# Kernel optimization log

Measured on AMD Instinct MI355X. Metric: run time of the kernel, lower is better.

## Reference

```python
import jax, jax.numpy as jnp
import numpy as np
from jax import lax

C = 64
EPS = 1e-6

def ln2d(x, w, b):
    # channel-wise LN over HxW per (n, c)
    mean = x.mean(axis=(2, 3), keepdims=True)
    var = ((x - mean) ** 2).mean(axis=(2, 3), keepdims=True)
    return (x - mean) / jnp.sqrt(var + EPS) * w + b

def pw(x, w, b):
    # 1x1 conv: w [O, I], b [O]
    return jnp.einsum('nihw,oi->nohw', x, w) + b[None, :, None, None]

def dwconv3(x, w, b):
    # depthwise 3x3, w [2C, 1, 3, 3]
    y = lax.conv_general_dilated(x, w, window_strides=(1, 1), padding='SAME',
                                 feature_group_count=x.shape[1],
                                 dimension_numbers=('NCHW', 'OIHW', 'NCHW'))
    return y + b[None, :, None, None]

def simple_gate(x):
    x1, x2 = jnp.split(x, 2, axis=1)
    return x1 * x2

def setup_inputs() -> dict:
    key = jax.random.key(0)
    ks = jax.random.split(key, 16)
    s = 0.05
    return {
        'x': jax.random.normal(ks[0], (8, C, 256, 256), jnp.float32),
        'ln1_w': jnp.ones((1, C, 1, 1), jnp.float32),
        'ln1_b': jnp.zeros((1, C, 1, 1), jnp.float32),
        'pw1_w': jax.random.normal(ks[1], (2 * C, C), jnp.float32) * s,
        'pw1_b': jnp.zeros((2 * C,), jnp.float32),
        'dw_w': jax.random.normal(ks[2], (2 * C, 1, 3, 3), jnp.float32) * s,
        'dw_b': jnp.zeros((2 * C,), jnp.float32),
        'sca_w': jax.random.normal(ks[3], (C, C), jnp.float32) * s,
        'sca_b': jnp.zeros((C,), jnp.float32),
        'pw2_w': jax.random.normal(ks[4], (C, C), jnp.float32) * s,
        'pw2_b': jnp.zeros((C,), jnp.float32),
        'ln2_w': jnp.ones((1, C, 1, 1), jnp.float32),
        'ln2_b': jnp.zeros((1, C, 1, 1), jnp.float32),
        'pw3_w': jax.random.normal(ks[5], (2 * C, C), jnp.float32) * s,
        'pw3_b': jnp.zeros((2 * C,), jnp.float32),
        'pw4_w': jax.random.normal(ks[6], (C, C), jnp.float32) * s,
        'pw4_b': jnp.zeros((C,), jnp.float32),
        'beta1': jax.random.normal(ks[7], (1, C, 1, 1), jnp.float32) * 0.1,
        'beta2': jax.random.normal(ks[8], (1, C, 1, 1), jnp.float32) * 0.1,
    }

def reference(x, ln1_w, ln1_b, pw1_w, pw1_b, dw_w, dw_b, sca_w, sca_b,
              pw2_w, pw2_b, ln2_w, ln2_b, pw3_w, pw3_b, pw4_w, pw4_b,
              beta1, beta2):
    y = ln2d(x, ln1_w, ln1_b)
    y = pw(y, pw1_w, pw1_b)
    y = dwconv3(y, dw_w, dw_b)
    y = simple_gate(y)
    # SCA: global avg pool -> 1x1 conv -> sigmoid scale
    s = y.mean(axis=(2, 3), keepdims=True)          # [N, C, 1, 1]
    w = jax.nn.sigmoid(pw(s, sca_w, sca_b))
    y = y * w
    y = pw(y, pw2_w, pw2_b)
    x = x + beta1 * y
    y2 = ln2d(x, ln2_w, ln2_b)
    y2 = pw(y2, pw3_w, pw3_b)
    y2 = simple_gate(y2)
    y2 = pw(y2, pw4_w, pw4_b)
    return x + beta2 * y2
```

## Files before the change

kernel.cpp:

```cpp
#include <hip/hip_runtime.h>
#include <hip/hip_bf16.h>

#define NB 8
#define HWP 65536
#define ZS  65664
#define TS  65664
#define XS  65600

typedef __attribute__((ext_vector_type(8))) short short8;
typedef __attribute__((ext_vector_type(4))) float f32x4;

__device__ __forceinline__ short f2bf(float f) {
  union { float f; unsigned u; } v; v.f = f;
  return (short)((v.u + 0x7FFF + ((v.u >> 16) & 1)) >> 16);
}
__device__ __forceinline__ float bf2f(unsigned short u) {
  union { unsigned u; float f; } v; v.u = ((unsigned)u) << 16; return v.f;
}

__global__ __launch_bounds__(512) void ln_stats_kernel(
    const float* __restrict__ x, const float* __restrict__ lw,
    const float* __restrict__ lb, float* __restrict__ a, float* __restrict__ b) {
  int plane = blockIdx.x;
  int c = plane & 63;
  const float4* p4 = (const float4*)(x + (size_t)plane * HWP);
  float s = 0.f, s2 = 0.f;
  for (int i = threadIdx.x; i < HWP / 4; i += 512) {
    float4 v = p4[i];
    s  += v.x + v.y + v.z + v.w;
    s2 += v.x * v.x + v.y * v.y + v.z * v.z + v.w * v.w;
  }
  for (int off = 32; off; off >>= 1) {
    s  += __shfl_down(s, off);
    s2 += __shfl_down(s2, off);
  }
  __shared__ float ls[8], ls2[8];
  int wid = threadIdx.x >> 6, lid = threadIdx.x & 63;
  if (lid == 0) { ls[wid] = s; ls2[wid] = s2; }
  __syncthreads();
  if (threadIdx.x == 0) {
    float S = 0.f, S2 = 0.f;
    for (int k = 0; k < 8; k++) { S += ls[k]; S2 += ls2[k]; }
    float mean = S * (1.f / (float)HWP);
    float var  = S2 * (1.f / (float)HWP) - mean * mean;
    float rstd = rsqrtf(var + 1e-6f);
    float av = rstd * lw[c];
    a[plane] = av;
    b[plane] = lb[c] - mean * av;
  }
}

__global__ void fold_kernel(const float* __restrict__ w, const float* __restrict__ pb,
                            const float* __restrict__ a, const float* __restrict__ b,
                            unsigned short* __restrict__ wf16, float* __restrict__ cf, int O) {
  int idx = blockIdx.x * blockDim.x + threadIdx.x;
  if (idx >= NB * O) return;
  int n = idx / O, o = idx - n * O;
  int MT = O >> 4;
  const float* an = a + n * 64;
  const float* bn = b + n * 64;
  const float* wo = w + o * 64;
  int mt = o >> 4, cl = o & 15;
  float cc = pb[o];
  for (int i = 0; i < 64; i++) {
    float wv = wo[i];
    float wf = wv * an[i];
    cc += wv * bn[i];
    int ks = i >> 5, quad = (i >> 3) & 3, j = i & 7;
    wf16[((((size_t)(n * MT + mt) * 2 + ks) * 16 + cl) * 4 + quad) * 8 + j] =
        (unsigned short)f2bf(wf);
  }
  cf[idx] = cc;
}

__global__ void fold4_kernel(const float* __restrict__ w4, const float* __restrict__ pb4,
                             const float* __restrict__ beta2,
                             unsigned short* __restrict__ wf16, float* __restrict__ cf) {
  int o = threadIdx.x;
  if (o >= 64) return;
  float bt = beta2[o];
  int mt = o >> 4, cl = o & 15;
  for (int i = 0; i < 64; i++) {
    int ks = i >> 5, quad = (i >> 3) & 3, j = i & 7;
    wf16[((((size_t)mt * 2 + ks) * 16 + cl) * 4 + quad) * 8 + j] =
        (unsigned short)f2bf(bt * w4[o * 64 + i]);
  }
  cf[o] = bt * pb4[o];
}

__global__ __launch_bounds__(256, 2) void gemm_pw1_kernel(
    const float* __restrict__ x, const unsigned short* __restrict__ wf16,
    const float* __restrict__ cf, unsigned short* __restrict__ z) {
  int n = blockIdx.y;
  int lane = threadIdx.x & 63, wid = threadIdx.x >> 6;
  int col = lane & 15, quad = lane >> 4;
  const short8* wv8 = (const short8*)wf16 + (size_t)n * 1024;
  short8 a[8][2];
  #pragma unroll
  for (int mt = 0; mt < 8; mt++)
    #pragma unroll
    for (int ks = 0; ks < 2; ks++)
      a[mt][ks] = wv8[((mt * 2 + ks) * 16 + col) * 4 + quad];
  f32x4 cb[8];
  #pragma unroll
  for (int mt = 0; mt < 8; mt++)
    cb[mt] = *(const f32x4*)(cf + n * 128 + mt * 16 + quad * 4);
  const float* xn = x + (size_t)n * 64 * HWP;
  unsigned short* zn = z + (size_t)n * 128 * ZS;
  int pxbase = blockIdx.x * 128 + wid * 16 + col;

  auto load_b = [&](int p, short8* bf) {
    #pragma unroll
    for (int ks = 0; ks < 2; ks++) {
      short8 v;
      #pragma unroll
      for (int j = 0; j < 8; j++)
        v[j] = f2bf(xn[(size_t)(ks * 32 + quad * 8 + j) * HWP + p]);
      bf[ks] = v;
    }
  };

  short8 bb[2][2];
  load_b(pxbase, bb[0]);
  #pragma unroll
  for (int tile = 0; tile < 2; tile++) {
    int cur = tile & 1, nxt = cur ^ 1;
    int p = pxbase + tile * 64;
    if (tile < 1) load_b(p + 64, bb[nxt]);
    f32x4 acc[8];
    #pragma unroll
    for (int mt = 0; mt < 8; mt++) {
      acc[mt] = cb[mt];
      acc[mt] = __builtin_amdgcn_mfma_f32_16x16x32_bf16(a[mt][0], bb[cur][0], acc[mt], 0, 0, 0);
      acc[mt] = __builtin_amdgcn_mfma_f32_16x16x32_bf16(a[mt][1], bb[cur][1], acc[mt], 0, 0, 0);
    }
    #pragma unroll
    for (int mt = 0; mt < 8; mt++)
      #pragma unroll
      for (int r = 0; r < 4; r++)
        zn[(size_t)(mt * 16 + quad * 4 + r) * ZS + p] =
            (unsigned short)f2bf(acc[mt][r]);
  }
}

__global__ __launch_bounds__(256) void dwgate_kernel(
    const unsigned short* __restrict__ z, const float* __restrict__ dww,
    const float* __restrict__ dwb, unsigned short* __restrict__ t,
    float* __restrict__ pooled4) {
  int blk = blockIdx.x;
  int plane = blk >> 2, qtr = blk & 3;
  int n = plane >> 6, c = plane & 63;
  int lane = threadIdx.x & 63, wv = threadIdx.x >> 6;
  const unsigned short* z0 = z + ((size_t)n * 128 + c) * ZS;
  const unsigned short* z1 = z0 + (size_t)64 * ZS;
  unsigned short* tp = t + (size_t)plane * TS;
  float w0[9], w1[9];
  #pragma unroll
  for (int k = 0; k < 9; k++) { w0[k] = dww[c * 9 + k]; w1[k] = dww[(c + 64) * 9 + k]; }
  float bias0 = dwb[c], bias1 = dwb[c + 64];
  int r0 = qtr * 64 + wv * 16;
  int colb = lane * 4;

  float fa[3][4], la[3], ra[3];
  float fb[3][4], lb_[3], rb[3];

  auto loadrow = [&](const unsigned short* base, int h, float* f, float& l, float& r) {
    if ((unsigned)h < 256u) {
      ushort4 u = *(const ushort4*)(base + h * 256 + colb);
      f[0] = bf2f(u.x); f[1] = bf2f(u.y); f[2] = bf2f(u.z); f[3] = bf2f(u.w);
    } else {
      f[0] = f[1] = f[2] = f[3] = 0.f;
    }
    float ll = __shfl_up(f[3], 1);
    float rr = __shfl_down(f[0], 1);
    l = (lane == 0) ? 0.f : ll;
    r = (lane == 63) ? 0.f : rr;
  };

  loadrow(z0, r0 - 1, fa[0], la[0], ra[0]);
  loadrow(z1, r0 - 1, fb[0], lb_[0], rb[0]);
  loadrow(z0, r0,     fa[1], la[1], ra[1]);
  loadrow(z1, r0,     fb[1], lb_[1], rb[1]);

  float lsum = 0.f;
  #pragma unroll 2
  for (int h = r0; h < r0 + 16; h++) {
    loadrow(z0, h + 1, fa[2], la[2], ra[2]);
    loadrow(z1, h + 1, fb[2], lb_[2], rb[2]);
    float o0[4] = {bias0, bias0, bias0, bias0};
    float o1[4] = {bias1, bias1, bias1, bias1};
    #pragma unroll
    for (int rr_ = 0; rr_ < 3; rr_++) {
      float wl0 = w0[rr_ * 3], wc0 = w0[rr_ * 3 + 1], wr0 = w0[rr_ * 3 + 2];
      float wl1 = w1[rr_ * 3], wc1 = w1[rr_ * 3 + 1], wr1 = w1[rr_ * 3 + 2];
      const float* f0 = fa[rr_]; const float* f1 = fb[rr_];
      float l0 = la[rr_], r0h = ra[rr_], l1 = lb_[rr_], r1h = rb[rr_];
      o0[0] += wl0 * l0    + wc0 * f0[0] + wr0 * f0[1];
      o0[1] += wl0 * f0[0] + wc0 * f0[1] + wr0 * f0[2];
      o0[2] += wl0 * f0[1] + wc0 * f0[2] + wr0 * f0[3];
      o0[3] += wl0 * f0[2] + wc0 * f0[3] + wr0 * r0h;
      o1[0] += wl1 * l1    + wc1 * f1[0] + wr1 * f1[1];
      o1[1] += wl1 * f1[0] + wc1 * f1[1] + wr1 * f1[2];
      o1[2] += wl1 * f1[1] + wc1 * f1[2] + wr1 * f1[3];
      o1[3] += wl1 * f1[2] + wc1 * f1[3] + wr1 * r1h;
    }
    float g0 = o0[0] * o1[0], g1 = o0[1] * o1[1];
    float g2 = o0[2] * o1[2], g3 = o0[3] * o1[3];
    uint2 pk;
    pk.x = (unsigned)(unsigned short)f2bf(g0) | ((unsigned)(unsigned short)f2bf(g1) << 16);
    pk.y = (unsigned)(unsigned short)f2bf(g2) | ((unsigned)(unsigned short)f2bf(g3) << 16);
    *(uint2*)(tp + (size_t)h * 256 + colb) = pk;
    lsum += (g0 + g1) + (g2 + g3);
    #pragma unroll
    for (int i = 0; i < 4; i++) { fa[0][i] = fa[1][i]; fa[1][i] = fa[2][i];
                                  fb[0][i] = fb[1][i]; fb[1][i] = fb[2][i]; }
    la[0] = la[1]; la[1] = la[2]; ra[0] = ra[1]; ra[1] = ra[2];
    lb_[0] = lb_[1]; lb_[1] = lb_[2]; rb[0] = rb[1]; rb[1] = rb[2];
  }
  for (int off = 32; off; off >>= 1) lsum += __shfl_down(lsum, off);
  __shared__ float ls[4];
  if (lane == 0) ls[wv] = lsum;
  __syncthreads();
  if (threadIdx.x == 0) pooled4[plane * 4 + qtr] = ls[0] + ls[1] + ls[2] + ls[3];
}

__global__ __launch_bounds__(256) void sca_fold_kernel(
    const float* __restrict__ pooled4, const float* __restrict__ sw,
    const float* __restrict__ sb, const float* __restrict__ w2,
    const float* __restrict__ pb2, const float* __restrict__ beta1,
    unsigned short* __restrict__ wf16, float* __restrict__ cf) {
  __shared__ float scal[4][64];
  int ln = threadIdx.x >> 6, o = threadIdx.x & 63;
  int n = blockIdx.x * 4 + ln;
  const float* pm = pooled4 + n * 256;
  float s = sb[o];
  for (int i = 0; i < 64; i++)
    s += sw[o * 64 + i] * (pm[i * 4] + pm[i * 4 + 1] + pm[i * 4 + 2] + pm[i * 4 + 3]) *
         (1.f / 65536.f);
  scal[ln][o] = 1.f / (1.f + expf(-s));
  __syncthreads();
  float bt = beta1[o];
  int mt = o >> 4, cl = o & 15;
  for (int i = 0; i < 64; i++) {
    float wf = bt * w2[o * 64 + i] * scal[ln][i];
    int ks = i >> 5, quad = (i >> 3) & 3, j = i & 7;
    wf16[((((size_t)(n * 4 + mt) * 2 + ks) * 16 + cl) * 4 + quad) * 8 + j] =
        (unsigned short)f2bf(wf);
  }
  cf[n * 64 + o] = bt * pb2[o];
}

__global__ __launch_bounds__(256, 2) void gemm_pw2_kernel(
    const unsigned short* __restrict__ t, const float* __restrict__ x,
    const unsigned short* __restrict__ wf16, const float* __restrict__ cf,
    float* __restrict__ x1, float* __restrict__ part_sum, float* __restrict__ part_sq) {
  __shared__ float red_s[4][64], red_q[4][64];
  int n = blockIdx.y;
  int lane = threadIdx.x & 63, wid = threadIdx.x >> 6;
  int col = lane & 15, quad = lane >> 4;
  const short8* wv8 = (const short8*)wf16 + (size_t)n * 512;
  short8 a[4][2];
  #pragma unroll
  for (int mt = 0; mt < 4; mt++)
    #pragma unroll
    for (int ks = 0; ks < 2; ks++)
      a[mt][ks] = wv8[((mt * 2 + ks) * 16 + col) * 4 + quad];
  f32x4 cb[4];
  #pragma unroll
  for (int mt = 0; mt < 4; mt++)
    cb[mt] = *(const f32x4*)(cf + n * 64 + mt * 16 + quad * 4);
  const unsigned short* tn = t + (size_t)n * 64 * TS;
  const float* xn = x + (size_t)n * 64 * HWP;
  float* x1n = x1 + (size_t)n * 64 * XS;
  int pxbase = blockIdx.x * 128 + wid * 16 + col;

  auto load_t = [&](int p, short8* bf) {
    #pragma unroll
    for (int ks = 0; ks < 2; ks++) {
      short8 v;
      #pragma unroll
      for (int j = 0; j < 8; j++)
        v[j] = (short)tn[(size_t)(ks * 32 + quad * 8 + j) * TS + p];
      bf[ks] = v;
    }
  };
  auto load_x = [&](int p, float (*xv)[4]) {
    #pragma unroll
    for (int mt = 0; mt < 4; mt++)
      #pragma unroll
      for (int r = 0; r < 4; r++)
        xv[mt][r] = xn[(size_t)(mt * 16 + quad * 4 + r) * HWP + p];
  };

  float sacc[4][4], qacc[4][4];
  #pragma unroll
  for (int mt = 0; mt < 4; mt++)
    #pragma unroll
    for (int r = 0; r < 4; r++) { sacc[mt][r] = 0.f; qacc[mt][r] = 0.f; }

  short8 bb[2][2];
  float xv[2][4][4];
  load_t(pxbase, bb[0]);
  load_x(pxbase, xv[0]);
  #pragma unroll
  for (int tile = 0; tile < 2; tile++) {
    int cur = tile & 1, nxt = cur ^ 1;
    int p = pxbase + tile * 64;
    if (tile < 1) { load_t(p + 64, bb[nxt]); load_x(p + 64, xv[nxt]); }
    f32x4 acc[4];
    #pragma unroll
    for (int mt = 0; mt < 4; mt++) {
      acc[mt] = cb[mt];
      acc[mt] = __builtin_amdgcn_mfma_f32_16x16x32_bf16(a[mt][0], bb[cur][0], acc[mt], 0, 0, 0);
      acc[mt] = __builtin_amdgcn_mfma_f32_16x16x32_bf16(a[mt][1], bb[cur][1], acc[mt], 0, 0, 0);
    }
    #pragma unroll
    for (int mt = 0; mt < 4; mt++)
      #pragma unroll
      for (int r = 0; r < 4; r++) {
        size_t idx = (size_t)(mt * 16 + quad * 4 + r) * XS + p;
        float v = xv[cur][mt][r] + acc[mt][r];
        x1n[idx] = v;
        sacc[mt][r] += v;
        qacc[mt][r] += v * v;
      }
  }
  #pragma unroll
  for (int mt = 0; mt < 4; mt++)
    #pragma unroll
    for (int r = 0; r < 4; r++) {
      float s = sacc[mt][r], q = qacc[mt][r];
      #pragma unroll
      for (int off = 1; off < 16; off <<= 1) {
        s += __shfl_xor(s, off);
        q += __shfl_xor(q, off);
      }
      if (col == 0) {
        int o = mt * 16 + quad * 4 + r;
        red_s[wid][o] = s; red_q[wid][o] = q;
      }
    }
  __syncthreads();
  if (threadIdx.x < 64) {
    int c = threadIdx.x;
    float s = red_s[0][c] + red_s[1][c] + red_s[2][c] + red_s[3][c];
    float q = red_q[0][c] + red_q[1][c] + red_q[2][c] + red_q[3][c];
    size_t pidx = ((size_t)n * 64 + c) * 512 + blockIdx.x;
    part_sum[pidx] = s;
    part_sq[pidx]  = q;
  }
}

__global__ __launch_bounds__(256) void ln2fold_kernel(
    const float* __restrict__ w, const float* __restrict__ pb,
    const float* __restrict__ ps, const float* __restrict__ pq,
    const float* __restrict__ lw, const float* __restrict__ lb,
    unsigned short* __restrict__ wf16, float* __restrict__ cf) {
  __shared__ float aa[64], bbv[64];
  int n = blockIdx.x;
  int c = threadIdx.x >> 2, k4 = threadIdx.x & 3;
  const float* p1 = ps + ((size_t)n * 64 + c) * 512 + k4 * 128;
  const float* p2 = pq + ((size_t)n * 64 + c) * 512 + k4 * 128;
  float S = 0.f, S2 = 0.f;
  for (int k = 0; k < 128; k++) { S += p1[k]; S2 += p2[k]; }
  S  += __shfl_xor(S, 1);  S  += __shfl_xor(S, 2);
  S2 += __shfl_xor(S2, 1); S2 += __shfl_xor(S2, 2);
  if (k4 == 0) {
    float mean = S * (1.f / (float)HWP);
    float var  = S2 * (1.f / (float)HWP) - mean * mean;
    float rstd = rsqrtf(var + 1e-6f);
    float av = rstd * lw[c];
    aa[c] = av;
    bbv[c] = lb[c] - mean * av;
  }
  __syncthreads();
  if (threadIdx.x < 128) {
    int o = threadIdx.x;
    const float* wo = w + o * 64;
    int mt = o >> 4, cl = o & 15;
    float cc = pb[o];
    for (int i = 0; i < 64; i++) {
      float wv = wo[i];
      float wf = wv * aa[i];
      cc += wv * bbv[i];
      int ks = i >> 5, quad = (i >> 3) & 3, j = i & 7;
      wf16[((((size_t)(n * 8 + mt) * 2 + ks) * 16 + cl) * 4 + quad) * 8 + j] =
          (unsigned short)f2bf(wf);
    }
    cf[n * 128 + o] = cc;
  }
}

__global__ __launch_bounds__(256, 2) void final_mfma_kernel(
    const float* __restrict__ x1, const unsigned short* __restrict__ w3f16,
    const float* __restrict__ c3f, const unsigned short* __restrict__ w4f16,
    const float* __restrict__ c4f, float* __restrict__ out) {
  __shared__ float s_c3[128];
  __shared__ __align__(16) float s_c4[64];
  int n = blockIdx.y;
  int lane = threadIdx.x & 63, wid = threadIdx.x >> 6;
  int col = lane & 15, quad = lane >> 4;
  if (threadIdx.x < 128) s_c3[threadIdx.x] = c3f[n * 128 + threadIdx.x];
  if (threadIdx.x < 64) s_c4[threadIdx.x] = c4f[threadIdx.x];
  const short8* w3v = (const short8*)w3f16 + (size_t)n * 1024;
  short8 a3[8][2];
  #pragma unroll
  for (int mt = 0; mt < 8; mt++)
    #pragma unroll
    for (int ks = 0; ks < 2; ks++)
      a3[mt][ks] = w3v[((mt * 2 + ks) * 16 + col) * 4 + quad];
  const short8* w4v = (const short8*)w4f16;
  short8 a4[4][2];
  #pragma unroll
  for (int mt = 0; mt < 4; mt++)
    #pragma unroll
    for (int ks = 0; ks < 2; ks++)
      a4[mt][ks] = w4v[((mt * 2 + ks) * 16 + col) * 4 + quad];
  __syncthreads();
  const float* x1n = x1 + (size_t)n * 64 * XS;
  float* outn = out + (size_t)n * 64 * HWP;
  int pxbase = blockIdx.x * 128 + wid * 16 + col;

  auto load_b1 = [&](int p, short8* bf) {
    #pragma unroll
    for (int ks = 0; ks < 2; ks++) {
      short8 v;
      #pragma unroll
      for (int j = 0; j < 8; j++)
        v[j] = f2bf(x1n[(size_t)(ks * 32 + quad * 8 + j) * XS + p]);
      bf[ks] = v;
    }
  };

  short8 bb1[2][2];
  load_b1(pxbase, bb1[0]);
  #pragma unroll
  for (int tile = 0; tile < 2; tile++) {
    int cur = tile & 1, nxt = cur ^ 1;
    int p = pxbase + tile * 64;
    if (tile < 1) load_b1(p + 64, bb1[nxt]);
    f32x4 acc[8];
    #pragma unroll
    for (int mt = 0; mt < 8; mt++) {
      acc[mt] = (f32x4){0.f, 0.f, 0.f, 0.f};
      acc[mt] = __builtin_amdgcn_mfma_f32_16x16x32_bf16(a3[mt][0], bb1[cur][0], acc[mt], 0, 0, 0);
      acc[mt] = __builtin_amdgcn_mfma_f32_16x16x32_bf16(a3[mt][1], bb1[cur][1], acc[mt], 0, 0, 0);
    }
    unsigned pd[4][2];
    #pragma unroll
    for (int mt = 0; mt < 4; mt++)
      #pragma unroll
      for (int u = 0; u < 2; u++) {
        int c0 = mt * 16 + quad * 4 + 2 * u;
        float ga = (acc[mt][2 * u]     + s_c3[c0])     * (acc[mt + 4][2 * u]     + s_c3[64 + c0]);
        float gb = (acc[mt][2 * u + 1] + s_c3[c0 + 1]) * (acc[mt + 4][2 * u + 1] + s_c3[64 + c0 + 1]);
        pd[mt][u] = (unsigned)(unsigned short)f2bf(ga) |
                    ((unsigned)(unsigned short)f2bf(gb) << 16);
      }
    short8 b2f[2];
    #pragma unroll
    for (int ks = 0; ks < 2; ks++)
      #pragma unroll
      for (int w = 0; w < 4; w++) {
        int src = ((quad & 1) * 2 + (w >> 1)) * 16 + col;
        unsigned v0 = (unsigned)__shfl((int)pd[ks * 2][w & 1], src, 64);
        unsigned v1 = (unsigned)__shfl((int)pd[ks * 2 + 1][w & 1], src, 64);
        unsigned u = (quad & 2) ? v1 : v0;
        b2f[ks][2 * w]     = (short)(u & 0xFFFFu);
        b2f[ks][2 * w + 1] = (short)(u >> 16);
      }
    f32x4 acc2[4];
    #pragma unroll
    for (int mt = 0; mt < 4; mt++) {
      acc2[mt] = *(const f32x4*)&s_c4[mt * 16 + quad * 4];
      acc2[mt] = __builtin_amdgcn_mfma_f32_16x16x32_bf16(a4[mt][0], b2f[0], acc2[mt], 0, 0, 0);
      acc2[mt] = __builtin_amdgcn_mfma_f32_16x16x32_bf16(a4[mt][1], b2f[1], acc2[mt], 0, 0, 0);
    }
    #pragma unroll
    for (int mt = 0; mt < 4; mt++)
      #pragma unroll
      for (int r = 0; r < 4; r++) {
        size_t idx = (size_t)(mt * 16 + quad * 4 + r) * XS + p;
        outn[(size_t)(mt * 16 + quad * 4 + r) * HWP + p] = x1n[idx] + acc2[mt][r];
      }
  }
}

extern "C" void kernel_launch(void* const* d_in, const int* in_sizes, int n_in,
                              void* d_out, int out_size, void* d_ws, size_t ws_size,
                              hipStream_t stream) {
  const float* x    = (const float*)d_in[0];
  const float* ln1w = (const float*)d_in[1];
  const float* ln1b = (const float*)d_in[2];
  const float* pw1w = (const float*)d_in[3];
  const float* pw1b = (const float*)d_in[4];
  const float* dww  = (const float*)d_in[5];
  const float* dwb  = (const float*)d_in[6];
  const float* scaw = (const float*)d_in[7];
  const float* scab = (const float*)d_in[8];
  const float* pw2w = (const float*)d_in[9];
  const float* pw2b = (const float*)d_in[10];
  const float* ln2w = (const float*)d_in[11];
  const float* ln2b = (const float*)d_in[12];
  const float* pw3w = (const float*)d_in[13];
  const float* pw3b = (const float*)d_in[14];
  const float* pw4w = (const float*)d_in[15];
  const float* pw4b = (const float*)d_in[16];
  const float* beta1= (const float*)d_in[17];
  const float* beta2= (const float*)d_in[18];
  float* out = (float*)d_out;

  char* ws = (char*)d_ws;
  unsigned short* z  = (unsigned short*)ws;
  float*          x1 = (float*)ws;
  unsigned short* t  = (unsigned short*)(ws + 134479872ull);
  float* sm = (float*)(ws + 134479872ull + 67239936ull);
  float* a1 = sm;
  float* b1 = a1 + 512;
  float* c1f = b1 + 512;
  float* pooled4 = c1f + 1024;
  float* c2f = pooled4 + 2048;
  float* c3f = c2f + 512;
  float* c4f = c3f + 1024;
  unsigned short* w1f16 = (unsigned short*)(c4f + 64);
  unsigned short* w2f16 = w1f16 + 65536;
  unsigned short* w3f16 = w2f16 + 32768;
  unsigned short* w4f16 = w3f16 + 65536;
  float* part_sum = (float*)d_out;
  float* part_sq  = part_sum + 262144;

  hipLaunchKernelGGL(ln_stats_kernel, dim3(512), dim3(512), 0, stream, x, ln1w, ln1b, a1, b1);
  hipLaunchKernelGGL(fold_kernel, dim3(4), dim3(256), 0, stream, pw1w, pw1b, a1, b1, w1f16, c1f, 128);
  hipLaunchKernelGGL(fold4_kernel, dim3(1), dim3(64), 0, stream, pw4w, pw4b, beta2, w4f16, c4f);
  hipLaunchKernelGGL(gemm_pw1_kernel, dim3(512, 8), dim3(256), 0, stream, x, w1f16, c1f, z);
  hipLaunchKernelGGL(dwgate_kernel, dim3(2048), dim3(256), 0, stream, z, dww, dwb, t, pooled4);
  hipLaunchKernelGGL(sca_fold_kernel, dim3(2), dim3(256), 0, stream,
                     pooled4, scaw, scab, pw2w, pw2b, beta1, w2f16, c2f);
  hipLaunchKernelGGL(gemm_pw2_kernel, dim3(512, 8), dim3(256), 0, stream, t, x, w2f16, c2f, x1,
                     part_sum, part_sq);
  hipLaunchKernelGGL(ln2fold_kernel, dim3(8), dim3(256), 0, stream,
                     pw3w, pw3b, part_sum, part_sq, ln2w, ln2b, w3f16, c3f);
  hipLaunchKernelGGL(final_mfma_kernel, dim3(512, 8), dim3(256), 0, stream,
                     x1, w3f16, c3f, w4f16, c4f, out);
}
```

Measured before the change: 562.2 us.

## Switch intermediates z, t, x1 to pixel-major channel-last layout

```diff
diff --git a/kernel.cpp b/kernel.cpp
--- a/kernel.cpp
+++ b/kernel.cpp
@@ -3,9 +3,6 @@
 
 #define NB 8
 #define HWP 65536
-#define ZS  65664
-#define TS  65664
-#define XS  65600
 
 typedef __attribute__((ext_vector_type(8))) short short8;
 typedef __attribute__((ext_vector_type(4))) float f32x4;
@@ -106,7 +103,7 @@
   for (int mt = 0; mt < 8; mt++)
     cb[mt] = *(const f32x4*)(cf + n * 128 + mt * 16 + quad * 4);
   const float* xn = x + (size_t)n * 64 * HWP;
-  unsigned short* zn = z + (size_t)n * 128 * ZS;
+  unsigned short* zn = z + (size_t)n * HWP * 128;
   int pxbase = blockIdx.x * 128 + wid * 16 + col;
 
   auto load_b = [&](int p, short8* bf) {
@@ -135,108 +132,103 @@
       acc[mt] = __builtin_amdgcn_mfma_f32_16x16x32_bf16(a[mt][1], bb[cur][1], acc[mt], 0, 0, 0);
     }
     #pragma unroll
-    for (int mt = 0; mt < 8; mt++)
-      #pragma unroll
-      for (int r = 0; r < 4; r++)
-        zn[(size_t)(mt * 16 + quad * 4 + r) * ZS + p] =
-            (unsigned short)f2bf(acc[mt][r]);
+    for (int mt = 0; mt < 8; mt++) {
+      uint2 pk;
+      pk.x = (unsigned)(unsigned short)f2bf(acc[mt][0]) |
+             ((unsigned)(unsigned short)f2bf(acc[mt][1]) << 16);
+      pk.y = (unsigned)(unsigned short)f2bf(acc[mt][2]) |
+             ((unsigned)(unsigned short)f2bf(acc[mt][3]) << 16);
+      *(uint2*)(zn + (size_t)p * 128 + mt * 16 + quad * 4) = pk;
+    }
   }
 }
 
 __global__ __launch_bounds__(256) void dwgate_kernel(
     const unsigned short* __restrict__ z, const float* __restrict__ dww,
     const float* __restrict__ dwb, unsigned short* __restrict__ t,
-    float* __restrict__ pooled4) {
+    float* __restrict__ pooledp) {
   int blk = blockIdx.x;
-  int plane = blk >> 2, qtr = blk & 3;
-  int n = plane >> 6, c = plane & 63;
-  int lane = threadIdx.x & 63, wv = threadIdx.x >> 6;
-  const unsigned short* z0 = z + ((size_t)n * 128 + c) * ZS;
-  const unsigned short* z1 = z0 + (size_t)64 * ZS;
-  unsigned short* tp = t + (size_t)plane * TS;
+  int n = blk >> 7, rem = blk & 127, s = rem >> 5, band = rem & 31;
+  int c = threadIdx.x & 63, w = threadIdx.x >> 6;
+  int cs = s * 64 + w * 16;
+  int r0 = band * 8;
+  const unsigned short* zn = z + (size_t)n * HWP * 128;
+  unsigned short* tn = t + (size_t)n * HWP * 64;
   float w0[9], w1[9];
   #pragma unroll
   for (int k = 0; k < 9; k++) { w0[k] = dww[c * 9 + k]; w1[k] = dww[(c + 64) * 9 + k]; }
   float bias0 = dwb[c], bias1 = dwb[c + 64];
-  int r0 = qtr * 64 + wv * 16;
-  int colb = lane * 4;
-
-  float fa[3][4], la[3], ra[3];
-  float fb[3][4], lb_[3], rb[3];
-
-  auto loadrow = [&](const unsigned short* base, int h, float* f, float& l, float& r) {
-    if ((unsigned)h < 256u) {
-      ushort4 u = *(const ushort4*)(base + h * 256 + colb);
-      f[0] = bf2f(u.x); f[1] = bf2f(u.y); f[2] = bf2f(u.z); f[3] = bf2f(u.w);
+  bool lok = (cs != 0);
+  bool rok = (cs + 16 < 256);
+
+  float wz[2][3][18];
+
+  auto loadrow = [&](int hh, int slot) {
+    if ((unsigned)hh < 256u) {
+      const unsigned short* rp = zn + (size_t)hh * 256 * 128 + c;
+      #pragma unroll
+      for (int m = 0; m < 18; m++) {
+        int px = cs - 1 + m;
+        bool ok = (m == 0) ? lok : ((m == 17) ? rok : true);
+        if (ok) {
+          wz[0][slot][m] = bf2f(rp[(size_t)px * 128]);
+          wz[1][slot][m] = bf2f(rp[(size_t)px * 128 + 64]);
+        } else {
+          wz[0][slot][m] = 0.f; wz[1][slot][m] = 0.f;
+        }
+      }
     } else {
-      f[0] = f[1] = f[2] = f[3] = 0.f;
-    }
-    float ll = __shfl_up(f[3], 1);
-    float rr = __shfl_down(f[0], 1);
-    l = (lane == 0) ? 0.f : ll;
-    r = (lane == 63) ? 0.f : rr;
+      #pragma unroll
+      for (int m = 0; m < 18; m++) { wz[0][slot][m] = 0.f; wz[1][slot][m] = 0.f; }
+    }
   };
 
-  loadrow(z0, r0 - 1, fa[0], la[0], ra[0]);
-  loadrow(z1, r0 - 1, fb[0], lb_[0], rb[0]);
-  loadrow(z0, r0,     fa[1], la[1], ra[1]);
-  loadrow(z1, r0,     fb[1], lb_[1], rb[1]);
-
+  loadrow(r0 - 1, 0);
+  loadrow(r0,     1);
   float lsum = 0.f;
-  #pragma unroll 2
-  for (int h = r0; h < r0 + 16; h++) {
-    loadrow(z0, h + 1, fa[2], la[2], ra[2]);
-    loadrow(z1, h + 1, fb[2], lb_[2], rb[2]);
-    float o0[4] = {bias0, bias0, bias0, bias0};
-    float o1[4] = {bias1, bias1, bias1, bias1};
-    #pragma unroll
-    for (int rr_ = 0; rr_ < 3; rr_++) {
-      float wl0 = w0[rr_ * 3], wc0 = w0[rr_ * 3 + 1], wr0 = w0[rr_ * 3 + 2];
-      float wl1 = w1[rr_ * 3], wc1 = w1[rr_ * 3 + 1], wr1 = w1[rr_ * 3 + 2];
-      const float* f0 = fa[rr_]; const float* f1 = fb[rr_];
-      float l0 = la[rr_], r0h = ra[rr_], l1 = lb_[rr_], r1h = rb[rr_];
-      o0[0] += wl0 * l0    + wc0 * f0[0] + wr0 * f0[1];
-      o0[1] += wl0 * f0[0] + wc0 * f0[1] + wr0 * f0[2];
-      o0[2] += wl0 * f0[1] + wc0 * f0[2] + wr0 * f0[3];
-      o0[3] += wl0 * f0[2] + wc0 * f0[3] + wr0 * r0h;
-      o1[0] += wl1 * l1    + wc1 * f1[0] + wr1 * f1[1];
-      o1[1] += wl1 * f1[0] + wc1 * f1[1] + wr1 * f1[2];
-      o1[2] += wl1 * f1[1] + wc1 * f1[2] + wr1 * f1[3];
-      o1[3] += wl1 * f1[2] + wc1 * f1[3] + wr1 * r1h;
-    }
-    float g0 = o0[0] * o1[0], g1 = o0[1] * o1[1];
-    float g2 = o0[2] * o1[2], g3 = o0[3] * o1[3];
-    uint2 pk;
-    pk.x = (unsigned)(unsigned short)f2bf(g0) | ((unsigned)(unsigned short)f2bf(g1) << 16);
-    pk.y = (unsigned)(unsigned short)f2bf(g2) | ((unsigned)(unsigned short)f2bf(g3) << 16);
-    *(uint2*)(tp + (size_t)h * 256 + colb) = pk;
-    lsum += (g0 + g1) + (g2 + g3);
-    #pragma unroll
-    for (int i = 0; i < 4; i++) { fa[0][i] = fa[1][i]; fa[1][i] = fa[2][i];
-                                  fb[0][i] = fb[1][i]; fb[1][i] = fb[2][i]; }
-    la[0] = la[1]; la[1] = la[2]; ra[0] = ra[1]; ra[1] = ra[2];
-    lb_[0] = lb_[1]; lb_[1] = lb_[2]; rb[0] = rb[1]; rb[1] = rb[2];
-  }
-  for (int off = 32; off; off >>= 1) lsum += __shfl_down(lsum, off);
-  __shared__ float ls[4];
-  if (lane == 0) ls[wv] = lsum;
-  __syncthreads();
-  if (threadIdx.x == 0) pooled4[plane * 4 + qtr] = ls[0] + ls[1] + ls[2] + ls[3];
+  #pragma unroll
+  for (int i = 0; i < 8; i++) {
+    const int sp = i % 3, sc = (i + 1) % 3, sn = (i + 2) % 3;
+    loadrow(r0 + i + 1, sn);
+    int hh = r0 + i;
+    #pragma unroll
+    for (int j = 0; j < 16; j++) {
+      float o0 = bias0, o1 = bias1;
+      o0 += w0[0] * wz[0][sp][j] + w0[1] * wz[0][sp][j + 1] + w0[2] * wz[0][sp][j + 2];
+      o0 += w0[3] * wz[0][sc][j] + w0[4] * wz[0][sc][j + 1] + w0[5] * wz[0][sc][j + 2];
+      o0 += w0[6] * wz[0][sn][j] + w0[7] * wz[0][sn][j + 1] + w0[8] * wz[0][sn][j + 2];
+      o1 += w1[0] * wz[1][sp][j] + w1[1] * wz[1][sp][j + 1] + w1[2] * wz[1][sp][j + 2];
+      o1 += w1[3] * wz[1][sc][j] + w1[4] * wz[1][sc][j + 1] + w1[5] * wz[1][sc][j + 2];
+      o1 += w1[6] * wz[1][sn][j] + w1[7] * wz[1][sn][j + 1] + w1[8] * wz[1][sn][j + 2];
+      float g = o0 * o1;
+      tn[(size_t)(hh * 256 + cs + j) * 64 + c] = (unsigned short)f2bf(g);
+      lsum += g;
+    }
+  }
+  __shared__ float red[4][64];
+  red[w][c] = lsum;
+  __syncthreads();
+  if (threadIdx.x < 64)
+    pooledp[((size_t)n * 128 + s * 32 + band) * 64 + threadIdx.x] =
+        red[0][threadIdx.x] + red[1][threadIdx.x] + red[2][threadIdx.x] + red[3][threadIdx.x];
 }
 
 __global__ __launch_bounds__(256) void sca_fold_kernel(
-    const float* __restrict__ pooled4, const float* __restrict__ sw,
+    const float* __restrict__ pooledp, const float* __restrict__ sw,
     const float* __restrict__ sb, const float* __restrict__ w2,
     const float* __restrict__ pb2, const float* __restrict__ beta1,
     unsigned short* __restrict__ wf16, float* __restrict__ cf) {
+  __shared__ float psum[4][64];
   __shared__ float scal[4][64];
   int ln = threadIdx.x >> 6, o = threadIdx.x & 63;
   int n = blockIdx.x * 4 + ln;
-  const float* pm = pooled4 + n * 256;
+  float S = 0.f;
+  for (int k = 0; k < 128; k++) S += pooledp[((size_t)n * 128 + k) * 64 + o];
+  psum[ln][o] = S;
+  __syncthreads();
   float s = sb[o];
   for (int i = 0; i < 64; i++)
-    s += sw[o * 64 + i] * (pm[i * 4] + pm[i * 4 + 1] + pm[i * 4 + 2] + pm[i * 4 + 3]) *
-         (1.f / 65536.f);
+    s += sw[o * 64 + i] * psum[ln][i] * (1.f / 65536.f);
   scal[ln][o] = 1.f / (1.f + expf(-s));
   __syncthreads();
   float bt = beta1[o];
@@ -269,20 +261,15 @@
   #pragma unroll
   for (int mt = 0; mt < 4; mt++)
     cb[mt] = *(const f32x4*)(cf + n * 64 + mt * 16 + quad * 4);
-  const unsigned short* tn = t + (size_t)n * 64 * TS;
+  const unsigned short* tn = t + (size_t)n * HWP * 64;
   const float* xn = x + (size_t)n * 64 * HWP;
-  float* x1n = x1 + (size_t)n * 64 * XS;
+  float* x1n = x1 + (size_t)n * HWP * 64;
   int pxbase = blockIdx.x * 128 + wid * 16 + col;
 
   auto load_t = [&](int p, short8* bf) {
     #pragma unroll
-    for (int ks = 0; ks < 2; ks++) {
-      short8 v;
-      #pragma unroll
-      for (int j = 0; j < 8; j++)
-        v[j] = (short)tn[(size_t)(ks * 32 + quad * 8 + j) * TS + p];
-      bf[ks] = v;
-    }
+    for (int ks = 0; ks < 2; ks++)
+      bf[ks] = *(const short8*)(tn + (size_t)p * 64 + ks * 32 + quad * 8);
   };
   auto load_x = [&](int p, float (*xv)[4]) {
     #pragma unroll
@@ -315,15 +302,18 @@
       acc[mt] = __builtin_amdgcn_mfma_f32_16x16x32_bf16(a[mt][1], bb[cur][1], acc[mt], 0, 0, 0);
     }
     #pragma unroll
-    for (int mt = 0; mt < 4; mt++)
+    for (int mt = 0; mt < 4; mt++) {
+      float4 st;
+      float* sv = (float*)&st;
       #pragma unroll
       for (int r = 0; r < 4; r++) {
-        size_t idx = (size_t)(mt * 16 + quad * 4 + r) * XS + p;
         float v = xv[cur][mt][r] + acc[mt][r];
-        x1n[idx] = v;
+        sv[r] = v;
         sacc[mt][r] += v;
         qacc[mt][r] += v * v;
       }
+      *(float4*)(x1n + (size_t)p * 64 + mt * 16 + quad * 4) = st;
+    }
   }
   #pragma unroll
   for (int mt = 0; mt < 4; mt++)
@@ -342,10 +332,10 @@
     }
   __syncthreads();
   if (threadIdx.x < 64) {
-    int c = threadIdx.x;
-    float s = red_s[0][c] + red_s[1][c] + red_s[2][c] + red_s[3][c];
-    float q = red_q[0][c] + red_q[1][c] + red_q[2][c] + red_q[3][c];
-    size_t pidx = ((size_t)n * 64 + c) * 512 + blockIdx.x;
+    int cc = threadIdx.x;
+    float s = red_s[0][cc] + red_s[1][cc] + red_s[2][cc] + red_s[3][cc];
+    float q = red_q[0][cc] + red_q[1][cc] + red_q[2][cc] + red_q[3][cc];
+    size_t pidx = ((size_t)n * 64 + cc) * 512 + blockIdx.x;
     part_sum[pidx] = s;
     part_sq[pidx]  = q;
   }
@@ -417,17 +407,18 @@
     for (int ks = 0; ks < 2; ks++)
       a4[mt][ks] = w4v[((mt * 2 + ks) * 16 + col) * 4 + quad];
   __syncthreads();
-  const float* x1n = x1 + (size_t)n * 64 * XS;
+  const float* x1n = x1 + (size_t)n * HWP * 64;
   float* outn = out + (size_t)n * 64 * HWP;
   int pxbase = blockIdx.x * 128 + wid * 16 + col;
 
   auto load_b1 = [&](int p, short8* bf) {
     #pragma unroll
     for (int ks = 0; ks < 2; ks++) {
+      float4 f0 = *(const float4*)(x1n + (size_t)p * 64 + ks * 32 + quad * 8);
+      float4 f1 = *(const float4*)(x1n + (size_t)p * 64 + ks * 32 + quad * 8 + 4);
       short8 v;
-      #pragma unroll
-      for (int j = 0; j < 8; j++)
-        v[j] = f2bf(x1n[(size_t)(ks * 32 + quad * 8 + j) * XS + p]);
+      v[0] = f2bf(f0.x); v[1] = f2bf(f0.y); v[2] = f2bf(f0.z); v[3] = f2bf(f0.w);
+      v[4] = f2bf(f1.x); v[5] = f2bf(f1.y); v[6] = f2bf(f1.z); v[7] = f2bf(f1.w);
       bf[ks] = v;
     }
   };
@@ -477,12 +468,13 @@
       acc2[mt] = __builtin_amdgcn_mfma_f32_16x16x32_bf16(a4[mt][1], b2f[1], acc2[mt], 0, 0, 0);
     }
     #pragma unroll
-    for (int mt = 0; mt < 4; mt++)
-      #pragma unroll
-      for (int r = 0; r < 4; r++) {
-        size_t idx = (size_t)(mt * 16 + quad * 4 + r) * XS + p;
-        outn[(size_t)(mt * 16 + quad * 4 + r) * HWP + p] = x1n[idx] + acc2[mt][r];
-      }
+    for (int mt = 0; mt < 4; mt++) {
+      float4 xr = *(const float4*)(x1n + (size_t)p * 64 + mt * 16 + quad * 4);
+      const float* xv = (const float*)&xr;
+      #pragma unroll
+      for (int r = 0; r < 4; r++)
+        outn[(size_t)(mt * 16 + quad * 4 + r) * HWP + p] = xv[r] + acc2[mt][r];
+    }
   }
 }
 
@@ -513,16 +505,16 @@
   char* ws = (char*)d_ws;
   unsigned short* z  = (unsigned short*)ws;
   float*          x1 = (float*)ws;
-  unsigned short* t  = (unsigned short*)(ws + 134479872ull);
-  float* sm = (float*)(ws + 134479872ull + 67239936ull);
+  unsigned short* t  = (unsigned short*)(ws + 134217728ull);
+  float* sm = (float*)(ws + 134217728ull + 67108864ull);
   float* a1 = sm;
   float* b1 = a1 + 512;
   float* c1f = b1 + 512;
-  float* pooled4 = c1f + 1024;
-  float* c2f = pooled4 + 2048;
+  float* c2f = c1f + 1024;
   float* c3f = c2f + 512;
   float* c4f = c3f + 1024;
-  unsigned short* w1f16 = (unsigned short*)(c4f + 64);
+  float* pooledp = c4f + 64;
+  unsigned short* w1f16 = (unsigned short*)(pooledp + 65536);
   unsigned short* w2f16 = w1f16 + 65536;
   unsigned short* w3f16 = w2f16 + 32768;
   unsigned short* w4f16 = w3f16 + 65536;
@@ -533,9 +525,9 @@
   hipLaunchKernelGGL(fold_kernel, dim3(4), dim3(256), 0, stream, pw1w, pw1b, a1, b1, w1f16, c1f, 128);
   hipLaunchKernelGGL(fold4_kernel, dim3(1), dim3(64), 0, stream, pw4w, pw4b, beta2, w4f16, c4f);
   hipLaunchKernelGGL(gemm_pw1_kernel, dim3(512, 8), dim3(256), 0, stream, x, w1f16, c1f, z);
-  hipLaunchKernelGGL(dwgate_kernel, dim3(2048), dim3(256), 0, stream, z, dww, dwb, t, pooled4);
+  hipLaunchKernelGGL(dwgate_kernel, dim3(1024), dim3(256), 0, stream, z, dww, dwb, t, pooledp);
   hipLaunchKernelGGL(sca_fold_kernel, dim3(2), dim3(256), 0, stream,
-                     pooled4, scaw, scab, pw2w, pw2b, beta1, w2f16, c2f);
+                     pooledp, scaw, scab, pw2w, pw2b, beta1, w2f16, c2f);
   hipLaunchKernelGGL(gemm_pw2_kernel, dim3(512, 8), dim3(256), 0, stream, t, x, w2f16, c2f, x1,
                      part_sum, part_sq);
   hipLaunchKernelGGL(ln2fold_kernel, dim3(8), dim3(256), 0, stream,
```

Result: slower. 599.9 us (+6.7%).
